# Kernel tuning notes

Measured on AMD Instinct MI355X. Metric: run time of the kernel, lower is better.

Reference implementation:

```python
import jax, jax.numpy as jnp
import numpy as np

B, A, N = 1024, 64, 256   # batch, n_agent, obs_shape
M = 128                    # thought_size
H = M // 2                 # bi-LSTM hidden per direction
ACT = 64                   # action_shape
E_ATT = 64                 # attention embedding
E1 = M                     # actor_1 embedding (defaults to thought_size)
E2 = M                     # actor_2 embedding
K = 8                      # agent_per_group
THRESH = 0.5
LN_EPS = 1e-5


def setup_inputs() -> dict:
    key = jax.random.key(0)
    ks = jax.random.split(key, 32)
    r = lambda k, shp, s=0.05: jax.random.normal(k, shp, jnp.float32) * s
    return {
        'obs': jax.random.normal(ks[0], (B, A, N), jnp.float32),
        # actor_1: Linear(N,E1) -> LayerNorm(E1) -> ReLU -> Linear(E1,M)
        'a1_w1': r(ks[1], (E1, N)), 'a1_b1': r(ks[2], (E1,)),
        'ln_g': jnp.ones((E1,), jnp.float32), 'ln_b': jnp.zeros((E1,), jnp.float32),
        'a1_w2': r(ks[3], (M, E1)), 'a1_b2': r(ks[4], (M,)),
        # attention unit: 3-layer MLP
        'att_w1': r(ks[5], (E_ATT, M)), 'att_b1': r(ks[6], (E_ATT,)),
        'att_w2': r(ks[7], (E_ATT, E_ATT)), 'att_b2': r(ks[8], (E_ATT,)),
        'att_w3': r(ks[9], (1, E_ATT)), 'att_b3': r(ks[10], (1,)),
        # bi-LSTM (torch gate order i,f,g,o), forward + backward directions
        'wih_f': r(ks[11], (4 * H, M)), 'whh_f': r(ks[12], (4 * H, H)),
        'bih_f': r(ks[13], (4 * H,)), 'bhh_f': r(ks[14], (4 * H,)),
        'wih_b': r(ks[15], (4 * H, M)), 'whh_b': r(ks[16], (4 * H, H)),
        'bih_b': r(ks[17], (4 * H,)), 'bhh_b': r(ks[18], (4 * H,)),
        # actor_2: ReLU -> Linear(2M,E2) -> Linear(E2,ACT,no bias) -> Tanh
        'a2_w1': r(ks[19], (E2, 2 * M)), 'a2_b1': r(ks[20], (E2,)),
        'a2_w2': r(ks[21], (ACT, E2)),
    }


def _lstm_dir(x, wih, whh, b):
    # x: (T, M) single sequence; returns (T, H)
    def cell(carry, xt):
        h, c = carry
        z = xt @ wih.T + h @ whh.T + b
        i, f, g, o = jnp.split(z, 4)
        c = jax.nn.sigmoid(f) * c + jax.nn.sigmoid(i) * jnp.tanh(g)
        h = jax.nn.sigmoid(o) * jnp.tanh(c)
        return (h, c), h
    init = (jnp.zeros((H,), x.dtype), jnp.zeros((H,), x.dtype))
    _, hs = jax.lax.scan(cell, init, x)
    return hs


def _bilstm(x, wih_f, whh_f, bf, wih_b, whh_b, bb):
    hf = _lstm_dir(x, wih_f, whh_f, bf)
    hb = _lstm_dir(x[::-1], wih_b, whh_b, bb)[::-1]
    return jnp.concatenate([hf, hb], axis=-1)  # (T, 2H) == (T, M)


def reference(obs, a1_w1, a1_b1, ln_g, ln_b, a1_w2, a1_b2,
              att_w1, att_b1, att_w2, att_b2, att_w3, att_b3,
              wih_f, whh_f, bih_f, bhh_f, wih_b, whh_b, bih_b, bhh_b,
              a2_w1, a2_b1, a2_w2):
    # ---- actor_1: obs -> thoughts ----
    h = obs @ a1_w1.T + a1_b1
    mu = h.mean(-1, keepdims=True)
    var = ((h - mu) ** 2).mean(-1, keepdims=True)
    h = (h - mu) * jax.lax.rsqrt(var + LN_EPS) * ln_g + ln_b
    thoughts = jax.nn.relu(h) @ a1_w2.T + a1_b2  # (B, A, M)

    # ---- attention unit: initiator probability ----
    a = jax.nn.relu(thoughts @ att_w1.T + att_b1)
    a = jax.nn.relu(a @ att_w2.T + att_b2)
    init_prob = jax.nn.sigmoid((a @ att_w3.T + att_b3)[..., 0])  # (B, A)
    is_init = init_prob > THRESH

    # ---- group formation: K nearest agents by squared distance ----
    dot = jnp.einsum('bim,bjm->bij', thoughts, thoughts)
    sq = jnp.einsum('bim,bim->bi', thoughts, thoughts)
    dists = sq[:, None, :] - 2.0 * dot + sq[:, :, None]  # (B, A, A)
    # torch scatters by ascending agent index (j-loop), so sort chosen indices
    idx = jnp.sort(jnp.argsort(dists, axis=-1)[..., :K], axis=-1)  # (B, A, K)

    # ---- sequential gather -> bi-LSTM -> scatter, per initiator in order ----
    bf, bb = bih_f + bhh_f, bih_b + bhh_b

    def update_one_batch(nt0, idx_b, init_b):
        def body(nt, inp):
            idx_i, init_i = inp
            gathered = nt[idx_i]                      # (K, M) from CURRENT state
            integ = _bilstm(gathered, wih_f, whh_f, bf, wih_b, whh_b, bb)
            upd = nt.at[idx_i].set(integ)
            return jnp.where(init_i, upd, nt), None
        nt, _ = jax.lax.scan(body, nt0, (idx_b, init_b))
        return nt

    new_thoughts = jax.vmap(update_one_batch)(thoughts, idx, is_init)  # (B, A, M)

    # ---- actor_2 ----
    x = jax.nn.relu(jnp.concatenate([thoughts, new_thoughts], axis=-1))
    x = x @ a2_w1.T + a2_b1
    action = jnp.tanh(x @ a2_w2.T)  # (B, A, ACT)
    return action


if __name__ == '__main__':
    out = reference(**setup_inputs())
    print(out.shape)
```

## Files before the change

kernel.cpp:

```cpp
#include <hip/hip_runtime.h>

typedef unsigned int u32;
typedef unsigned short u16;
typedef unsigned long long u64;
typedef _Float16 h2 __attribute__((ext_vector_type(2)));
typedef _Float16 h4 __attribute__((ext_vector_type(4)));
typedef _Float16 h8 __attribute__((ext_vector_type(8)));
typedef float f4 __attribute__((ext_vector_type(4)));

#define ROWS 65536
#define NB 1024
#define NA 64

__device__ __forceinline__ float dot4(float4 w, float4 x){
  return w.x*x.x + w.y*x.y + w.z*x.z + w.w*x.w;
}
__device__ __forceinline__ h2 u32_h2(u32 v){ union { u32 u; h2 h; } x; x.u = v; return x.h; }
__device__ __forceinline__ h2 pack_h2(float a, float b){ h2 r; r.x = (_Float16)a; r.y = (_Float16)b; return r; }
__device__ __forceinline__ h4 pack_h4(float4 v){
  h4 r; r.x=(_Float16)v.x; r.y=(_Float16)v.y; r.z=(_Float16)v.z; r.w=(_Float16)v.w; return r;
}
__device__ __forceinline__ h4 pack_h4_relu(float4 v){
  h4 r; r.x=(_Float16)fmaxf(v.x,0.f); r.y=(_Float16)fmaxf(v.y,0.f);
  r.z=(_Float16)fmaxf(v.z,0.f); r.w=(_Float16)fmaxf(v.w,0.f); return r;
}
__device__ __forceinline__ float fsig(float z){
  float e = __builtin_amdgcn_exp2f(-1.44269504f * z);
  return __builtin_amdgcn_rcpf(1.0f + e);
}
__device__ __forceinline__ float ftanh(float z){
  float e = __builtin_amdgcn_exp2f(2.885390082f * z);
  return 1.0f - 2.0f * __builtin_amdgcn_rcpf(1.0f + e);
}
__device__ __forceinline__ h8 load8f(const float* p){
  float4 a = *(const float4*)p;
  float4 b = *(const float4*)(p + 4);
  h8 r;
  r[0] = (_Float16)a.x; r[1] = (_Float16)a.y; r[2] = (_Float16)a.z; r[3] = (_Float16)a.w;
  r[4] = (_Float16)b.x; r[5] = (_Float16)b.y; r[6] = (_Float16)b.z; r[7] = (_Float16)b.w;
  return r;
}

__global__ __launch_bounds__(256) void k_cvt(
    const float* __restrict__ a2w1, const float* __restrict__ a2w2,
    _Float16* __restrict__ w1h, _Float16* __restrict__ w2h)
{
  int i = blockIdx.x * 256 + threadIdx.x;
  if (i < 32768) w1h[i] = (_Float16)a2w1[i];
  if (i < 8192)  w2h[i] = (_Float16)a2w2[i];
}

__global__ __launch_bounds__(128) void k_actor1(
    const float* __restrict__ obs, const float* __restrict__ w1, const float* __restrict__ b1,
    const float* __restrict__ lng, const float* __restrict__ lnb,
    const float* __restrict__ w2, const float* __restrict__ b2,
    const float* __restrict__ aw1, const float* __restrict__ ab1,
    const float* __restrict__ aw2, const float* __restrict__ ab2,
    const float* __restrict__ aw3, const float* __restrict__ ab3,
    float* __restrict__ thoughts, int* __restrict__ isinit)
{
  const int b0 = blockIdx.x * 8;
  const int t = threadIdx.x;
  __shared__ float4 xs[8][64];
  __shared__ float hs[8][128];
  __shared__ float tb[8][128];
  __shared__ float ab[8][64];
  __shared__ float a2b[8][64];
  __shared__ float red[8][4];

  { const float4* og = (const float4*)(obs + (size_t)b0 * 256);
    #pragma unroll
    for (int j = 0; j < 4; j++){ int p = j * 128 + t; xs[p >> 6][p & 63] = og[p]; } }
  __syncthreads();

  float acc[8];
  #pragma unroll
  for (int r = 0; r < 8; r++) acc[r] = b1[t];
  { const float4* wr = (const float4*)(w1 + (size_t)t * 256);
    for (int j = 0; j < 64; j++){
      float4 w = wr[j];
      #pragma unroll
      for (int r = 0; r < 8; r++) acc[r] += dot4(w, xs[r][j]);
    } }

  #pragma unroll
  for (int r = 0; r < 8; r++){
    float s = acc[r], s2 = acc[r] * acc[r];
    #pragma unroll
    for (int off = 32; off > 0; off >>= 1){ s += __shfl_down(s, off); s2 += __shfl_down(s2, off); }
    if ((t & 63) == 0){ red[r][t >> 6] = s; red[r][2 + (t >> 6)] = s2; }
  }
  __syncthreads();
  const float g_ = lng[t], bb_ = lnb[t];
  #pragma unroll
  for (int r = 0; r < 8; r++){
    float mu  = (red[r][0] + red[r][1]) * (1.0f/128.0f);
    float var = (red[r][2] + red[r][3]) * (1.0f/128.0f) - mu * mu;
    hs[r][t] = fmaxf((acc[r] - mu) * rsqrtf(var + 1e-5f) * g_ + bb_, 0.0f);
  }
  __syncthreads();

  float acc2[8];
  #pragma unroll
  for (int r = 0; r < 8; r++) acc2[r] = b2[t];
  { const float4* wr = (const float4*)(w2 + (size_t)t * 128);
    for (int j = 0; j < 32; j++){
      float4 w = wr[j];
      #pragma unroll
      for (int r = 0; r < 8; r++) acc2[r] += dot4(w, ((const float4*)hs[r])[j]);
    } }
  #pragma unroll
  for (int r = 0; r < 8; r++){
    thoughts[(size_t)(b0 + r) * 128 + t] = acc2[r];
    tb[r][t] = acc2[r];
  }
  __syncthreads();

  if (t < 64){
    float a[8];
    #pragma unroll
    for (int r = 0; r < 8; r++) a[r] = ab1[t];
    const float4* wr = (const float4*)(aw1 + (size_t)t * 128);
    for (int j = 0; j < 32; j++){
      float4 w = wr[j];
      #pragma unroll
      for (int r = 0; r < 8; r++) a[r] += dot4(w, ((const float4*)tb[r])[j]);
    }
    #pragma unroll
    for (int r = 0; r < 8; r++) ab[r][t] = fmaxf(a[r], 0.0f);
  }
  __syncthreads();
  if (t < 64){
    float a[8];
    #pragma unroll
    for (int r = 0; r < 8; r++) a[r] = ab2[t];
    const float4* wr = (const float4*)(aw2 + (size_t)t * 64);
    for (int j = 0; j < 16; j++){
      float4 w = wr[j];
      #pragma unroll
      for (int r = 0; r < 8; r++) a[r] += dot4(w, ((const float4*)ab[r])[j]);
    }
    #pragma unroll
    for (int r = 0; r < 8; r++) a2b[r][t] = fmaxf(a[r], 0.0f);
  }
  __syncthreads();
  if (t < 8){
    float p = ab3[0];
    for (int j = 0; j < 64; j++) p += aw3[j] * a2b[t][j];
    isinit[b0 + t] = (p > 0.0f) ? 1 : 0;
  }
}

__global__ __launch_bounds__(256) void k_groups(
    const float* __restrict__ thoughts, int* __restrict__ idxout)
{
  const int b = blockIdx.x;
  const int tid = threadIdx.x;
  __shared__ float T[64 * 130];
  __shared__ float sq[64];
  for (int p = tid; p < 8192; p += 256){
    T[(p >> 7) * 130 + (p & 127)] = thoughts[(size_t)b * 8192 + p];
  }
  __syncthreads();
  if (tid < 64){
    const float2* tj = (const float2*)&T[tid * 130];
    float s = 0.0f;
    #pragma unroll 8
    for (int k = 0; k < 64; k++){ float2 v = tj[k]; s += v.x*v.x + v.y*v.y; }
    sq[tid] = s;
  }
  __syncthreads();
  const int lane = tid & 63;
  const int wv = tid >> 6;
  const float2* tj = (const float2*)&T[lane * 130];
  const float sqj = sq[lane];
  for (int ii = 0; ii < 16; ii++){
    const int i = wv * 16 + ii;
    const float2* ti = (const float2*)&T[i * 130];
    float dot = 0.0f;
    #pragma unroll 8
    for (int k = 0; k < 64; k++){ float2 a = ti[k]; float2 c = tj[k]; dot += a.x*c.x + a.y*c.y; }
    float d = fmaxf(sq[i] + sqj - 2.0f*dot, 0.0f);
    u64 key = (((u64)__float_as_uint(d)) << 32) | (u32)lane;
    u64 mask = 0;
    for (int q = 0; q < 8; q++){
      u64 m = key;
      #pragma unroll
      for (int off = 32; off > 0; off >>= 1){ u64 o = __shfl_xor(m, off); if (o < m) m = o; }
      mask |= 1ull << (u32)(m & 63u);
      if (key == m) key = ~0ull;
    }
    if (lane == 0){
      u64 mm = mask;
      int base = (b * 64 + i) * 8;
      #pragma unroll
      for (int q = 0; q < 8; q++){ int j = (int)__builtin_ctzll(mm); mm &= mm - 1; idxout[base + q] = j; }
    }
  }
}

__global__ __launch_bounds__(512, 2) void k_scan(
    const float* __restrict__ thoughts, const int* __restrict__ isinit, const int* __restrict__ idx,
    const float* __restrict__ wihf, const float* __restrict__ whhf,
    const float* __restrict__ bihf, const float* __restrict__ bhhf,
    const float* __restrict__ wihb, const float* __restrict__ whhb,
    const float* __restrict__ bihb, const float* __restrict__ bhhb,
    float* __restrict__ newt)
{
  const int b0   = blockIdx.x * 4;
  const int tid  = threadIdx.x;
  const int w    = tid >> 6;
  const int lane = tid & 63;
  const int dir  = w >> 2;
  const int wsub = w & 3;
  const int lr   = lane & 15;
  const int hi   = lane >> 4;

  __shared__ __align__(16) _Float16 nt16[4][64 * 136];
  __shared__ __align__(16) _Float16 Zx16[4][2*8*64*4];
  __shared__ __align__(16) _Float16 hb16[4][2][72];
  __shared__ int gall[4][512];
  __shared__ int flags[4][64];
  __shared__ int dirty[4][64];

  const float* wih = dir ? wihb : wihf;
  const float* whh = dir ? whhb : whhf;

  h8 Bf[4][4];
  #pragma unroll
  for (int ni = 0; ni < 4; ni++){
    const float* wr = wih + (size_t)((wsub << 6) + (ni << 4) + lr) * 128 + (hi << 3);
    #pragma unroll
    for (int kt = 0; kt < 4; kt++) Bf[ni][kt] = load8f(wr + kt * 32);
    __builtin_amdgcn_sched_barrier(0);
  }
  h8 Bh[4][2];
  #pragma unroll
  for (int gg = 0; gg < 4; gg++){
    const float* wr = whh + (size_t)((gg << 6) + (wsub << 4) + lr) * 64 + (hi << 3);
    #pragma unroll
    for (int kt = 0; kt < 2; kt++) Bh[gg][kt] = load8f(wr + kt * 32);
    __builtin_amdgcn_sched_barrier(0);
  }
  float biasl[4];
  {
    const float* bih = dir ? bihb : bihf;
    const float* bhh = dir ? bhhb : bhhf;
    #pragma unroll
    for (int ni = 0; ni < 4; ni++){
      int n = (wsub << 6) + (ni << 4) + lr;
      biasl[ni] = bih[n] + bhh[n];
    }
  }

  #pragma unroll
  for (int q = 0; q < 4; q++){
    const float4* tf4 = (const float4*)(thoughts + (size_t)(b0 + q) * 8192);
    #pragma unroll
    for (int k2 = 0; k2 < 4; k2++){
      int id4 = tid + k2 * 512;
      float4 v = tf4[id4];
      *(h4*)&nt16[q][(id4 >> 5) * 136 + (id4 & 31) * 4] = pack_h4(v);
    }
  }
  #pragma unroll
  for (int k2 = 0; k2 < 4; k2++){
    int p = tid + k2 * 512;
    gall[p >> 9][p & 511] = idx[(size_t)b0 * 512 + p];
  }
  if (tid < 256){ int q = tid >> 6, j = tid & 63;
    flags[q][j] = isinit[(b0 + q) * 64 + j]; dirty[q][j] = 0; }
  if (tid < 288) ((h2*)hb16)[tid] = pack_h2(0.0f, 0.0f);
  __syncthreads();

  #pragma unroll 1
  for (int i = 0; i < 64; i++){
    const int f0 = flags[0][i], f1 = flags[1][i], f2 = flags[2][i], f3 = flags[3][i];
    if (!(f0 | f1 | f2 | f3)) continue;
    if (tid < 32){ int q = tid >> 3, j = tid & 7;
      int fq = (q == 0) ? f0 : (q == 1) ? f1 : (q == 2) ? f2 : f3;
      if (fq) dirty[q][gall[q][i * 8 + j]] = 1; }

    #pragma unroll
    for (int pr = 0; pr < 2; pr++){
      const int fp = pr ? (f2 | f3) : (f0 | f1);
      if (fp){
        const int qa = (pr << 1) + (lr >> 3);
        const int grow = gall[qa][i * 8 + (lr & 7)];
        h8 Af[4];
        #pragma unroll
        for (int kt = 0; kt < 4; kt++)
          Af[kt] = *(const h8*)&nt16[qa][grow * 136 + kt * 32 + (hi << 3)];
        const int qo = (pr << 1) + (hi >> 1), t0 = (hi & 1) << 2;
        #pragma unroll
        for (int ni = 0; ni < 4; ni++){
          f4 acc = {0.0f, 0.0f, 0.0f, 0.0f};
          #pragma unroll
          for (int kt = 0; kt < 4; kt++)
            acc = __builtin_amdgcn_mfma_f32_16x16x32_f16(Af[kt], Bf[ni][kt], acc, 0, 0, 0);
          const int lp = (ni << 4) + lr;
          #pragma unroll
          for (int r = 0; r < 4; r++)
            Zx16[qo][(((dir << 3) + t0 + r) * 64 + lp) * 4 + wsub] = (_Float16)(acc[r] + biasl[ni]);
        }
      }
    }
    __syncthreads();

    float c0 = 0.0f, c1 = 0.0f, c2 = 0.0f, c3 = 0.0f;
    #pragma unroll
    for (int s = 0; s < 8; s++){
      const int tt = dir ? (7 - s) : s;
      const int zoff = (((dir << 3) + tt) * 64 + (wsub << 4) + lr) * 4;
      uint2 zr0 = {0u,0u}, zr1 = {0u,0u}, zr2 = {0u,0u}, zr3 = {0u,0u};
      if (f0) zr0 = *(const uint2*)&Zx16[0][zoff];
      if (f1) zr1 = *(const uint2*)&Zx16[1][zoff];
      if (f2) zr2 = *(const uint2*)&Zx16[2][zoff];
      if (f3) zr3 = *(const uint2*)&Zx16[3][zoff];
      f4 A0, A1, A2, A3;
      { h2 pa = u32_h2(zr0.x), pb = u32_h2(zr0.y);
        A0[0] = (float)pa.x; A1[0] = (float)pa.y; A2[0] = (float)pb.x; A3[0] = (float)pb.y; }
      { h2 pa = u32_h2(zr1.x), pb = u32_h2(zr1.y);
        A0[1] = (float)pa.x; A1[1] = (float)pa.y; A2[1] = (float)pb.x; A3[1] = (float)pb.y; }
      { h2 pa = u32_h2(zr2.x), pb = u32_h2(zr2.y);
        A0[2] = (float)pa.x; A1[2] = (float)pa.y; A2[2] = (float)pb.x; A3[2] = (float)pb.y; }
      { h2 pa = u32_h2(zr3.x), pb = u32_h2(zr3.y);
        A0[3] = (float)pa.x; A1[3] = (float)pa.y; A2[3] = (float)pb.x; A3[3] = (float)pb.y; }
      if (s > 0){
        const int qa = lr & 3;
        h8 a0 = *(const h8*)&hb16[qa][dir][(hi << 3)];
        h8 a1 = *(const h8*)&hb16[qa][dir][32 + (hi << 3)];
        A0 = __builtin_amdgcn_mfma_f32_16x16x32_f16(a0, Bh[0][0], A0, 0, 0, 0);
        A0 = __builtin_amdgcn_mfma_f32_16x16x32_f16(a1, Bh[0][1], A0, 0, 0, 0);
        A1 = __builtin_amdgcn_mfma_f32_16x16x32_f16(a0, Bh[1][0], A1, 0, 0, 0);
        A1 = __builtin_amdgcn_mfma_f32_16x16x32_f16(a1, Bh[1][1], A1, 0, 0, 0);
        A2 = __builtin_amdgcn_mfma_f32_16x16x32_f16(a0, Bh[2][0], A2, 0, 0, 0);
        A2 = __builtin_amdgcn_mfma_f32_16x16x32_f16(a1, Bh[2][1], A2, 0, 0, 0);
        A3 = __builtin_amdgcn_mfma_f32_16x16x32_f16(a0, Bh[3][0], A3, 0, 0, 0);
        A3 = __builtin_amdgcn_mfma_f32_16x16x32_f16(a1, Bh[3][1], A3, 0, 0, 0);
      }
      #pragma unroll
      for (int q = 0; q < 4; q++){
        const int fq = (q == 0) ? f0 : (q == 1) ? f1 : (q == 2) ? f2 : f3;
        if (!fq) continue;
        float z0 = A0[q], z1 = A1[q], z2 = A2[q], z3 = A3[q];
        float fi = fsig(z0);
        float ff = fsig(z1);
        float fg = ftanh(z2);
        float fo = fsig(z3);
        float cc = (q == 0) ? c0 : (q == 1) ? c1 : (q == 2) ? c2 : c3;
        cc = ff * cc + fi * fg;
        if (q == 0) c0 = cc; else if (q == 1) c1 = cc; else if (q == 2) c2 = cc; else c3 = cc;
        float hn = fo * ftanh(cc);
        if (hi == 0){
          hb16[q][dir][(wsub << 4) + lr] = (_Float16)hn;
          nt16[q][gall[q][i * 8 + tt] * 136 + (dir << 6) + (wsub << 4) + lr] = (_Float16)hn;
        }
      }
      __syncthreads();
    }
  }

  __syncthreads();
  #pragma unroll
  for (int q = 0; q < 4; q++){
    const float4* tf4 = (const float4*)(thoughts + (size_t)(b0 + q) * 8192);
    float4* of4 = (float4*)(newt + (size_t)(b0 + q) * 8192);
    #pragma unroll
    for (int k2 = 0; k2 < 4; k2++){
      int id4 = tid + k2 * 512;
      int row = id4 >> 5, c4 = (id4 & 31) * 4;
      float4 v = tf4[id4];
      if (dirty[q][row]){
        h4 hv = *(const h4*)&nt16[q][row * 136 + c4];
        v.x = (float)hv.x; v.y = (float)hv.y; v.z = (float)hv.z; v.w = (float)hv.w;
      }
      of4[id4] = v;
    }
  }
}

__global__ __launch_bounds__(256) void k_actor2(
    const float* __restrict__ thoughts, const float* __restrict__ newt,
    const _Float16* __restrict__ w1h, const float* __restrict__ b1,
    const _Float16* __restrict__ w2h, float* __restrict__ out)
{
  const int b0 = blockIdx.x * 32;
  const int tid = threadIdx.x;
  const int w = tid >> 6, lane = tid & 63, lr = lane & 15, hi = lane >> 4;
  const int mt = w & 1, nb = (w >> 1) << 6;

  __shared__ __align__(16) _Float16 Xc[32 * 264];
  __shared__ __align__(16) _Float16 Ys[32 * 136];

  #pragma unroll
  for (int k2 = 0; k2 < 8; k2++){
    int id4 = tid + k2 * 256;
    int row = id4 >> 6, c4 = (id4 & 63) * 4;
    const float* src = (c4 < 128) ? (thoughts + (size_t)(b0 + row) * 128 + c4)
                                  : (newt + (size_t)(b0 + row) * 128 + (c4 - 128));
    float4 v = *(const float4*)src;
    *(h4*)&Xc[row * 264 + c4] = pack_h4_relu(v);
  }
  __syncthreads();

  {
    h8 Af[8];
    #pragma unroll
    for (int kt = 0; kt < 8; kt++)
      Af[kt] = *(const h8*)&Xc[(mt * 16 + lr) * 264 + kt * 32 + (hi << 3)];
    #pragma unroll
    for (int ni = 0; ni < 4; ni++){
      const int n = nb + ni * 16 + lr;
      const _Float16* wr = w1h + (size_t)n * 256 + (hi << 3);
      f4 acc = {0.0f, 0.0f, 0.0f, 0.0f};
      #pragma unroll
      for (int kt = 0; kt < 8; kt++){
        h8 bfr = *(const h8*)(wr + kt * 32);
        acc = __builtin_amdgcn_mfma_f32_16x16x32_f16(Af[kt], bfr, acc, 0, 0, 0);
      }
      const float bb = b1[n];
      #pragma unroll
      for (int r = 0; r < 4; r++){
        int row = mt * 16 + (hi << 2) + r;
        Ys[row * 136 + n] = (_Float16)(acc[r] + bb);
      }
    }
  }
  __syncthreads();

  {
    const int ni0 = (w >> 1) << 1;
    h8 Ag[4];
    #pragma unroll
    for (int kt = 0; kt < 4; kt++)
      Ag[kt] = *(const h8*)&Ys[(mt * 16 + lr) * 136 + kt * 32 + (hi << 3)];
    #pragma unroll
    for (int nj = 0; nj < 2; nj++){
      const int n = (ni0 + nj) * 16 + lr;
      const _Float16* wr = w2h + (size_t)n * 128 + (hi << 3);
      f4 acc = {0.0f, 0.0f, 0.0f, 0.0f};
      #pragma unroll
      for (int kt = 0; kt < 4; kt++){
        h8 bfr = *(const h8*)(wr + kt * 32);
        acc = __builtin_amdgcn_mfma_f32_16x16x32_f16(Ag[kt], bfr, acc, 0, 0, 0);
      }
      #pragma unroll
      for (int r = 0; r < 4; r++){
        int row = mt * 16 + (hi << 2) + r;
        out[(size_t)(b0 + row) * 64 + n] = ftanh(acc[r]);
      }
    }
  }
}

extern "C" void kernel_launch(void* const* d_in, const int* in_sizes, int n_in,
                              void* d_out, int out_size, void* d_ws, size_t ws_size,
                              hipStream_t stream)
{
  const float* obs  = (const float*)d_in[0];
  const float* w1   = (const float*)d_in[1];
  const float* b1   = (const float*)d_in[2];
  const float* lng  = (const float*)d_in[3];
  const float* lnb  = (const float*)d_in[4];
  const float* w2   = (const float*)d_in[5];
  const float* b2   = (const float*)d_in[6];
  const float* aw1  = (const float*)d_in[7];
  const float* ab1  = (const float*)d_in[8];
  const float* aw2  = (const float*)d_in[9];
  const float* ab2  = (const float*)d_in[10];
  const float* aw3  = (const float*)d_in[11];
  const float* ab3  = (const float*)d_in[12];
  const float* wihf = (const float*)d_in[13];
  const float* whhf = (const float*)d_in[14];
  const float* bihf = (const float*)d_in[15];
  const float* bhhf = (const float*)d_in[16];
  const float* wihb = (const float*)d_in[17];
  const float* whhb = (const float*)d_in[18];
  const float* bihb = (const float*)d_in[19];
  const float* bhhb = (const float*)d_in[20];
  const float* a2w1 = (const float*)d_in[21];
  const float* a2b1 = (const float*)d_in[22];
  const float* a2w2 = (const float*)d_in[23];

  float* thoughts = (float*)d_ws;
  float* newt     = thoughts + (size_t)ROWS * 128;
  int*   isinit   = (int*)(newt + (size_t)ROWS * 128);
  int*   idxb     = isinit + ROWS;
  _Float16* w1h   = (_Float16*)(idxb + (size_t)ROWS * 8);
  _Float16* w2h   = w1h + 32768;

  hipLaunchKernelGGL(k_cvt, dim3(128), dim3(256), 0, stream, a2w1, a2w2, w1h, w2h);
  hipLaunchKernelGGL(k_actor1, dim3(ROWS / 8), dim3(128), 0, stream,
                     obs, w1, b1, lng, lnb, w2, b2, aw1, ab1, aw2, ab2, aw3, ab3,
                     thoughts, isinit);
  hipLaunchKernelGGL(k_groups, dim3(NB), dim3(256), 0, stream, thoughts, idxb);
  hipLaunchKernelGGL(k_scan, dim3(NB / 4), dim3(512), 0, stream,
                     thoughts, isinit, idxb,
                     wihf, whhf, bihf, bhhf, wihb, whhb, bihb, bhhb, newt);
  hipLaunchKernelGGL(k_actor2, dim3(ROWS / 32), dim3(256), 0, stream,
                     thoughts, newt, w1h, a2b1, w2h, (float*)d_out);
}
```

Before: 909.9 us.

## Spread LSTM gate math across lane groups and keep input projections in fp32

In the scan kernel, each 16-lane group (hi) now computes the LSTM cell update for one batch slot, instead of every lane looping over all four slots and only hi==0 lanes writing. This cuts the serial transcendental work per lane by four. The precomputed input-gate buffer moves from fp16 to fp32 so it can be read with float4 loads without unpacking, which doubles that shared-memory buffer and may lower occupancy. The attention MLP in the first kernel also uses all 128 threads, splitting the 8 rows into two halves instead of idling half the block.

```diff
diff --git a/kernel.cpp b/kernel.cpp
--- a/kernel.cpp
+++ b/kernel.cpp
@@ -116,32 +116,33 @@
   }
   __syncthreads();
 
-  if (t < 64){
-    float a[8];
-    #pragma unroll
-    for (int r = 0; r < 8; r++) a[r] = ab1[t];
-    const float4* wr = (const float4*)(aw1 + (size_t)t * 128);
+  const int rh = t >> 6, fa = t & 63;
+  {
+    float a[4];
+    #pragma unroll
+    for (int r = 0; r < 4; r++) a[r] = ab1[fa];
+    const float4* wr = (const float4*)(aw1 + (size_t)fa * 128);
     for (int j = 0; j < 32; j++){
       float4 w = wr[j];
       #pragma unroll
-      for (int r = 0; r < 8; r++) a[r] += dot4(w, ((const float4*)tb[r])[j]);
-    }
-    #pragma unroll
-    for (int r = 0; r < 8; r++) ab[r][t] = fmaxf(a[r], 0.0f);
-  }
-  __syncthreads();
-  if (t < 64){
-    float a[8];
-    #pragma unroll
-    for (int r = 0; r < 8; r++) a[r] = ab2[t];
-    const float4* wr = (const float4*)(aw2 + (size_t)t * 64);
+      for (int r = 0; r < 4; r++) a[r] += dot4(w, ((const float4*)tb[rh * 4 + r])[j]);
+    }
+    #pragma unroll
+    for (int r = 0; r < 4; r++) ab[rh * 4 + r][fa] = fmaxf(a[r], 0.0f);
+  }
+  __syncthreads();
+  {
+    float a[4];
+    #pragma unroll
+    for (int r = 0; r < 4; r++) a[r] = ab2[fa];
+    const float4* wr = (const float4*)(aw2 + (size_t)fa * 64);
     for (int j = 0; j < 16; j++){
       float4 w = wr[j];
       #pragma unroll
-      for (int r = 0; r < 8; r++) a[r] += dot4(w, ((const float4*)ab[r])[j]);
-    }
-    #pragma unroll
-    for (int r = 0; r < 8; r++) a2b[r][t] = fmaxf(a[r], 0.0f);
+      for (int r = 0; r < 4; r++) a[r] += dot4(w, ((const float4*)ab[rh * 4 + r])[j]);
+    }
+    #pragma unroll
+    for (int r = 0; r < 4; r++) a2b[rh * 4 + r][fa] = fmaxf(a[r], 0.0f);
   }
   __syncthreads();
   if (t < 8){
@@ -217,7 +218,7 @@
   const int hi   = lane >> 4;
 
   __shared__ __align__(16) _Float16 nt16[4][64 * 136];
-  __shared__ __align__(16) _Float16 Zx16[4][2*8*64*4];
+  __shared__ __align__(16) float Zx32[4][2*8*64*4];
   __shared__ __align__(16) _Float16 hb16[4][2][72];
   __shared__ int gall[4][512];
   __shared__ int flags[4][64];
@@ -301,31 +302,26 @@
           const int lp = (ni << 4) + lr;
           #pragma unroll
           for (int r = 0; r < 4; r++)
-            Zx16[qo][(((dir << 3) + t0 + r) * 64 + lp) * 4 + wsub] = (_Float16)(acc[r] + biasl[ni]);
+            Zx32[qo][(((dir << 3) + t0 + r) * 64 + lp) * 4 + wsub] = acc[r] + biasl[ni];
         }
       }
     }
     __syncthreads();
 
-    float c0 = 0.0f, c1 = 0.0f, c2 = 0.0f, c3 = 0.0f;
+    float c = 0.0f;
+    const int fq = (hi == 0) ? f0 : (hi == 1) ? f1 : (hi == 2) ? f2 : f3;
     #pragma unroll
     for (int s = 0; s < 8; s++){
       const int tt = dir ? (7 - s) : s;
       const int zoff = (((dir << 3) + tt) * 64 + (wsub << 4) + lr) * 4;
-      uint2 zr0 = {0u,0u}, zr1 = {0u,0u}, zr2 = {0u,0u}, zr3 = {0u,0u};
-      if (f0) zr0 = *(const uint2*)&Zx16[0][zoff];
-      if (f1) zr1 = *(const uint2*)&Zx16[1][zoff];
-      if (f2) zr2 = *(const uint2*)&Zx16[2][zoff];
-      if (f3) zr3 = *(const uint2*)&Zx16[3][zoff];
-      f4 A0, A1, A2, A3;
-      { h2 pa = u32_h2(zr0.x), pb = u32_h2(zr0.y);
-        A0[0] = (float)pa.x; A1[0] = (float)pa.y; A2[0] = (float)pb.x; A3[0] = (float)pb.y; }
-      { h2 pa = u32_h2(zr1.x), pb = u32_h2(zr1.y);
-        A0[1] = (float)pa.x; A1[1] = (float)pa.y; A2[1] = (float)pb.x; A3[1] = (float)pb.y; }
-      { h2 pa = u32_h2(zr2.x), pb = u32_h2(zr2.y);
-        A0[2] = (float)pa.x; A1[2] = (float)pa.y; A2[2] = (float)pb.x; A3[2] = (float)pb.y; }
-      { h2 pa = u32_h2(zr3.x), pb = u32_h2(zr3.y);
-        A0[3] = (float)pa.x; A1[3] = (float)pa.y; A2[3] = (float)pb.x; A3[3] = (float)pb.y; }
+      float4 zq0 = *(const float4*)&Zx32[0][zoff];
+      float4 zq1 = *(const float4*)&Zx32[1][zoff];
+      float4 zq2 = *(const float4*)&Zx32[2][zoff];
+      float4 zq3 = *(const float4*)&Zx32[3][zoff];
+      f4 A0 = {zq0.x, zq1.x, zq2.x, zq3.x};
+      f4 A1 = {zq0.y, zq1.y, zq2.y, zq3.y};
+      f4 A2 = {zq0.z, zq1.z, zq2.z, zq3.z};
+      f4 A3 = {zq0.w, zq1.w, zq2.w, zq3.w};
       if (s > 0){
         const int qa = lr & 3;
         h8 a0 = *(const h8*)&hb16[qa][dir][(hi << 3)];
@@ -339,23 +335,19 @@
         A3 = __builtin_amdgcn_mfma_f32_16x16x32_f16(a0, Bh[3][0], A3, 0, 0, 0);
         A3 = __builtin_amdgcn_mfma_f32_16x16x32_f16(a1, Bh[3][1], A3, 0, 0, 0);
       }
-      #pragma unroll
-      for (int q = 0; q < 4; q++){
-        const int fq = (q == 0) ? f0 : (q == 1) ? f1 : (q == 2) ? f2 : f3;
-        if (!fq) continue;
-        float z0 = A0[q], z1 = A1[q], z2 = A2[q], z3 = A3[q];
-        float fi = fsig(z0);
-        float ff = fsig(z1);
-        float fg = ftanh(z2);
-        float fo = fsig(z3);
-        float cc = (q == 0) ? c0 : (q == 1) ? c1 : (q == 2) ? c2 : c3;
-        cc = ff * cc + fi * fg;
-        if (q == 0) c0 = cc; else if (q == 1) c1 = cc; else if (q == 2) c2 = cc; else c3 = cc;
-        float hn = fo * ftanh(cc);
-        if (hi == 0){
-          hb16[q][dir][(wsub << 4) + lr] = (_Float16)hn;
-          nt16[q][gall[q][i * 8 + tt] * 136 + (dir << 6) + (wsub << 4) + lr] = (_Float16)hn;
-        }
+      float z0 = (hi == 0) ? A0[0] : (hi == 1) ? A0[1] : (hi == 2) ? A0[2] : A0[3];
+      float z1 = (hi == 0) ? A1[0] : (hi == 1) ? A1[1] : (hi == 2) ? A1[2] : A1[3];
+      float z2 = (hi == 0) ? A2[0] : (hi == 1) ? A2[1] : (hi == 2) ? A2[2] : A2[3];
+      float z3 = (hi == 0) ? A3[0] : (hi == 1) ? A3[1] : (hi == 2) ? A3[2] : A3[3];
+      float fi = fsig(z0);
+      float ff = fsig(z1);
+      float fg = ftanh(z2);
+      float fo = fsig(z3);
+      c = ff * c + fi * fg;
+      float hn = fo * ftanh(c);
+      if (fq){
+        hb16[hi][dir][(wsub << 4) + lr] = (_Float16)hn;
+        nt16[hi][gall[hi][i * 8 + tt] * 136 + (dir << 6) + (wsub << 4) + lr] = (_Float16)hn;
       }
       __syncthreads();
     }
```

Result: faster. 884.9 us (-2.7%).
